# Optimization experiments

Hardware: AMD Instinct MI355X
Metric: run time of the kernel (lower is better)

The kernel has to match this reference:

```python
import jax, jax.numpy as jnp
import numpy as np

D = 1024           # input_size
D2 = 2 * D         # hidden width of the three inner linears
OUT = 1024         # output_size
S = 8192           # tokens per example


def setup_inputs() -> dict:
    key = jax.random.key(0)
    ks = jax.random.split(key, 11)
    def lin(k, fan_in, fan_out):
        bound = 1.0 / np.sqrt(fan_in)
        kw, kb = jax.random.split(k)
        W = jax.random.uniform(kw, (fan_in, fan_out), jnp.float32, -bound, bound)
        b = jax.random.uniform(kb, (fan_out,), jnp.float32, -bound, bound)
        return W, b
    W_in, b_in = lin(ks[0], D, D2)      # reading_example_input
    W_out, b_out = lin(ks[1], D, D2)    # reading_example_output
    W_cat, b_cat = lin(ks[2], D2, D2)   # concatenated_layer_map
    W_fin, b_fin = lin(ks[3], D2, OUT)  # final_map
    return {
        "input_embedding": jax.random.normal(ks[4], (1, S, D), jnp.float32),
        "output_embedding": jax.random.normal(ks[5], (1, S, D), jnp.float32),
        "random_augmentation": jax.random.normal(ks[6], (1, S, D), jnp.float32),
        "W_in": W_in, "b_in": b_in,
        "W_out": W_out, "b_out": b_out,
        "W_cat": W_cat, "b_cat": b_cat,
        "W_fin": W_fin, "b_fin": b_fin,
    }


def reference(input_embedding, output_embedding, random_augmentation,
              W_in, b_in, W_out, b_out, W_cat, b_cat, W_fin, b_fin):
    def march(x, y):
        # x, y: [1, S, D]
        iq = jax.nn.softmax(x @ W_in + b_in, axis=-1)[0]    # [S, 2D]
        oq = jax.nn.softmax(y @ W_out + b_out, axis=-1)[0]  # [S, 2D]
        cat = jnp.concatenate((x, y), axis=-1)[0]           # [S, 2D]
        icm = jax.nn.softmax(cat @ W_cat + b_cat, axis=-1)  # [S, 2D]
        iqk = iq.T @ icm                                    # [2D, 2D]
        oqk = oq.T @ icm                                    # [2D, 2D]
        meta = jax.nn.relu(iqk @ oqk.T)                     # [2D, 2D]
        scale = jnp.sqrt(jnp.float32(icm.shape[-1]))
        res = (icm @ meta) / scale                          # [S, 2D]
        return jax.nn.relu(res @ W_fin + b_fin)             # [S, OUT]

    transformation = march(input_embedding, output_embedding)
    random_desc = march(input_embedding, random_augmentation)
    return (transformation, random_desc)
```

## Files before the change

### kernel.cpp

```cpp
#include <hip/hip_runtime.h>

#define S_TOK 8192
#define DIM   1024
#define DIM2  2048
#define OUTN  1024

typedef __bf16 bf16x8 __attribute__((ext_vector_type(8)));
typedef float  f32x4  __attribute__((ext_vector_type(4)));
typedef short  s16x8  __attribute__((ext_vector_type(8)));
typedef unsigned short u16x4 __attribute__((ext_vector_type(4)));

__device__ __forceinline__ unsigned short f2bf(float x) {
  unsigned u = __builtin_bit_cast(unsigned, x);
  u = (u + 0x7FFFu + ((u >> 16) & 1u)) >> 16;
  return (unsigned short)u;
}
__device__ __forceinline__ float bf2f(unsigned short u) {
  return __builtin_bit_cast(float, (unsigned)u << 16);
}

__device__ __forceinline__ void gld_lds16(const void* g, void* l) {
  auto* g1 = reinterpret_cast<__attribute__((address_space(1))) unsigned*>(
      (unsigned long long)g);
  auto* l3 = reinterpret_cast<__attribute__((address_space(3))) unsigned*>(
      (unsigned long long)l);
  __builtin_amdgcn_global_load_lds(g1, l3, 16, 0, 0);
}

__device__ __forceinline__ int lds_off(int idx, int k) {
  int b = (idx << 7) + (k << 1);
  b ^= ((idx ^ (idx >> 3)) & 7) << 4;
  return b;
}

__global__ __launch_bounds__(256) void cvt_f32_bf16(const float* __restrict__ in,
                                                    unsigned short* __restrict__ out, int n4) {
  int i = blockIdx.x * 256 + threadIdx.x;
  if (i >= n4) return;
  float4 v = ((const float4*)in)[i];
  u16x4 o;
  o[0] = f2bf(v.x); o[1] = f2bf(v.y); o[2] = f2bf(v.z); o[3] = f2bf(v.w);
  *(u16x4*)(out + (size_t)i * 4) = o;
}

template <int F32IN>
__global__ __launch_bounds__(256) void transpose_to_bf16(const void* __restrict__ in,
                                                         unsigned short* __restrict__ out,
                                                         int R, int C) {
  __shared__ unsigned short t[64 * 64];
  const int r0 = blockIdx.y << 6, c0 = blockIdx.x << 6;
  const int tid = threadIdx.x;
#pragma unroll
  for (int i = 0; i < 2; ++i) {
    int ch = tid + (i << 8);
    int r = ch >> 3, c8 = (ch & 7) << 3;
    s16x8 w;
    if (F32IN) {
      const float* p = (const float*)in + (size_t)(r0 + r) * C + c0 + c8;
      float4 a = *(const float4*)p, b = *(const float4*)(p + 4);
      w[0] = (short)f2bf(a.x); w[1] = (short)f2bf(a.y);
      w[2] = (short)f2bf(a.z); w[3] = (short)f2bf(a.w);
      w[4] = (short)f2bf(b.x); w[5] = (short)f2bf(b.y);
      w[6] = (short)f2bf(b.z); w[7] = (short)f2bf(b.w);
    } else {
      w = *(const s16x8*)((const unsigned short*)in + (size_t)(r0 + r) * C + c0 + c8);
    }
    int sw = ((r ^ (r >> 3)) & 7) << 3;
    *(s16x8*)&t[(r << 6) + (c8 ^ sw)] = w;
  }
  __syncthreads();
#pragma unroll
  for (int i = 0; i < 2; ++i) {
    int ch = tid + (i << 8);
    int c = ch >> 3, r8 = (ch & 7) << 3;
    s16x8 w;
#pragma unroll
    for (int j = 0; j < 8; ++j) {
      int rr = r8 + j;
      w[j] = (short)t[(rr << 6) + (c ^ (((rr ^ (rr >> 3)) & 7) << 3))];
    }
    *(s16x8*)(out + (size_t)(c0 + c) * R + r0 + r8) = w;
  }
}

struct SmTab { unsigned short* T[6]; };
__global__ __launch_bounds__(512) void softmax_cols(SmTab tab) {
  unsigned short* T = tab.T[blockIdx.y];
  const int tid = threadIdx.x;
  const int colg = tid & 63, seg = tid >> 6;
  const size_t c = ((size_t)blockIdx.x << 6) + colg;
  float m = -1e30f, s = 0.f;
  for (int n = seg; n < DIM2; n += 8) {
    float v = bf2f(T[(size_t)n * S_TOK + c]);
    float mn = fmaxf(m, v);
    s = s * __expf(m - mn) + __expf(v - mn);
    m = mn;
  }
  __shared__ float redm[512], reds[512];
  redm[tid] = m; reds[tid] = s;
  __syncthreads();
  if (seg == 0) {
    float M = m, S = s;
#pragma unroll
    for (int k = 1; k < 8; ++k) {
      float mk = redm[colg + (k << 6)], sk = reds[colg + (k << 6)];
      float mn = fmaxf(M, mk);
      S = S * __expf(M - mn) + sk * __expf(mk - mn);
      M = mn;
    }
    redm[colg] = M; reds[colg] = 1.0f / S;
  }
  __syncthreads();
  m = redm[colg];
  const float inv = reds[colg];
  for (int n = seg; n < DIM2; n += 8) {
    size_t idx = (size_t)n * S_TOK + c;
    T[idx] = f2bf(__expf(bf2f(T[idx]) - m) * inv);
  }
}

struct GPtr {
  const unsigned short* A[3];
  const unsigned short* Arow2[3];
  const unsigned short* B[3];
  const unsigned short* Bk2[3];
  const float* bias[3];
  void* C[3];
};
template <int ASPLIT, int BSPLIT, int BIAS_ROW, int OUT_BF16>
__global__ __launch_bounds__(256, 3) void gemm_nt(GPtr p, int lda, int ldb, int ldc,
                                                  int K, float scale, int do_relu) {
  __shared__ char lds[32768];
  char* As = lds;
  char* Bs = lds + 16384;
  const int z = blockIdx.z;
  const int tid  = threadIdx.x;
  const int lane = tid & 63;
  const int wave = tid >> 6;
  const int wm = (wave >> 1) << 6;
  const int wn = (wave & 1) << 6;
  const int m0 = blockIdx.y << 7;
  const int n0 = blockIdx.x << 7;

  const unsigned short* Au = p.A[z];
  int mb = m0;
  if (ASPLIT && m0 >= 2048) { Au = p.Arow2[z]; mb = m0 - 2048; }
  const unsigned short* B  = p.B[z];
  const unsigned short* B2 = BSPLIT ? p.Bk2[z] : B;
  const float* bias = p.bias[z];
  void* Cv = p.C[z];

  int srow[4], sgk[4];
#pragma unroll
  for (int i = 0; i < 4; ++i) {
    int c = (wave << 8) + (i << 6) + lane;
    int row = c >> 3, kc = c & 7;
    srow[i] = row;
    sgk[i]  = (kc ^ ((row ^ (row >> 3)) & 7)) << 3;
  }

  f32x4 acc[4][4];
#pragma unroll
  for (int i = 0; i < 4; ++i)
#pragma unroll
    for (int j = 0; j < 4; ++j) acc[i][j] = {0.f, 0.f, 0.f, 0.f};

  for (int k0 = 0; k0 < K; k0 += 64) {
    const unsigned short* bsrc = B;
    int kb = k0;
    if (BSPLIT && k0 >= DIM) { bsrc = B2; kb = k0 - DIM; }
#pragma unroll
    for (int i = 0; i < 4; ++i) {
      char* dA = As + (((wave << 2) + i) << 10);
      char* dB = Bs + (((wave << 2) + i) << 10);
      gld_lds16(Au   + (size_t)(mb + srow[i]) * lda + k0 + sgk[i], dA);
      gld_lds16(bsrc + (size_t)(n0 + srow[i]) * ldb + kb + sgk[i], dB);
    }
    __syncthreads();
#pragma unroll
    for (int ks = 0; ks < 2; ++ks) {
      bf16x8 af[4], bfr[4];
      int kk = (ks << 5) + ((lane >> 4) << 3);
#pragma unroll
      for (int t = 0; t < 4; ++t) {
        af[t]  = *(const bf16x8*)(As + lds_off(wm + (t << 4) + (lane & 15), kk));
        bfr[t] = *(const bf16x8*)(Bs + lds_off(wn + (t << 4) + (lane & 15), kk));
      }
#pragma unroll
      for (int mt = 0; mt < 4; ++mt)
#pragma unroll
        for (int nt = 0; nt < 4; ++nt)
          acc[mt][nt] = __builtin_amdgcn_mfma_f32_16x16x32_bf16(af[mt], bfr[nt], acc[mt][nt], 0, 0, 0);
    }
    __syncthreads();
  }

#pragma unroll
  for (int nt = 0; nt < 4; ++nt) {
    int col = n0 + wn + (nt << 4) + (lane & 15);
    float bcol = (!BIAS_ROW && bias) ? bias[col] : 0.0f;
#pragma unroll
    for (int mt = 0; mt < 4; ++mt) {
      f32x4 a = acc[mt][nt];
#pragma unroll
      for (int r = 0; r < 4; ++r) {
        int rowg = m0 + wm + (mt << 4) + ((lane >> 4) << 2) + r;
        float bv = BIAS_ROW ? (bias ? bias[rowg] : 0.0f) : bcol;
        float v = a[r] * scale + bv;
        if (do_relu) v = fmaxf(v, 0.0f);
        if (OUT_BF16) ((unsigned short*)Cv)[(size_t)rowg * ldc + col] = f2bf(v);
        else          ((float*)Cv)[(size_t)rowg * ldc + col] = v;
      }
    }
  }
}

extern "C" void kernel_launch(void* const* d_in, const int* in_sizes, int n_in,
                              void* d_out, int out_size, void* d_ws, size_t ws_size,
                              hipStream_t stream) {
  const float* X   = (const float*)d_in[0];
  const float* Y   = (const float*)d_in[1];
  const float* R   = (const float*)d_in[2];
  const float* Wi  = (const float*)d_in[3];
  const float* bi  = (const float*)d_in[4];
  const float* Wo  = (const float*)d_in[5];
  const float* bo  = (const float*)d_in[6];
  const float* Wc  = (const float*)d_in[7];
  const float* bc  = (const float*)d_in[8];
  const float* Wf  = (const float*)d_in[9];
  const float* bf_ = (const float*)d_in[10];
  float* out = (float*)d_out;

  char* ws = (char*)d_ws;
  size_t off = 0;
  auto alloc = [&](size_t b) { char* p = ws + off; off += (b + 255) & ~(size_t)255; return p; };
  unsigned short* Xb   = (unsigned short*)alloc((size_t)S_TOK * DIM  * 2);
  unsigned short* Yb   = (unsigned short*)alloc((size_t)S_TOK * DIM  * 2);
  unsigned short* Rb   = (unsigned short*)alloc((size_t)S_TOK * DIM  * 2);
  unsigned short* WiT  = (unsigned short*)alloc((size_t)DIM2 * DIM  * 2);
  unsigned short* WoT  = (unsigned short*)alloc((size_t)DIM2 * DIM  * 2);
  unsigned short* WcT  = (unsigned short*)alloc((size_t)DIM2 * DIM2 * 2);
  unsigned short* WfT  = (unsigned short*)alloc((size_t)OUTN * DIM2 * 2);
  unsigned short* iqT  = (unsigned short*)alloc((size_t)DIM2 * S_TOK * 2);
  unsigned short* oqT0 = (unsigned short*)alloc((size_t)DIM2 * S_TOK * 2);
  unsigned short* oqT1 = (unsigned short*)alloc((size_t)DIM2 * S_TOK * 2);
  unsigned short* icmT0= (unsigned short*)alloc((size_t)DIM2 * S_TOK * 2);
  unsigned short* icmT1= (unsigned short*)alloc((size_t)DIM2 * S_TOK * 2);
  unsigned short* iqk0 = Xb;
  unsigned short* oqk0 = Xb + (size_t)DIM2*DIM2;
  unsigned short* iqk1 = Yb;
  unsigned short* oqk1 = Yb + (size_t)DIM2*DIM2;
  unsigned short* meta0= iqT;
  unsigned short* meta1= iqT + (size_t)DIM2*DIM2;
  unsigned short* MWT0 = iqT + (size_t)2*DIM2*DIM2;
  unsigned short* MWT1 = iqT + (size_t)2*DIM2*DIM2 + (size_t)OUTN*DIM2;
  unsigned short* icm0 = oqT0;
  unsigned short* icm1 = oqT1;

  auto cvt = [&](const float* s, unsigned short* d, int n) {
    int n4 = n >> 2;
    cvt_f32_bf16<<<dim3((n4 + 255) / 256), dim3(256), 0, stream>>>(s, d, n4);
  };
  cvt(X, Xb, S_TOK * DIM);
  cvt(Y, Yb, S_TOK * DIM);
  cvt(R, Rb, S_TOK * DIM);
  transpose_to_bf16<1><<<dim3(DIM2 / 64, DIM  / 64), 256, 0, stream>>>(Wi, WiT, DIM,  DIM2);
  transpose_to_bf16<1><<<dim3(DIM2 / 64, DIM  / 64), 256, 0, stream>>>(Wo, WoT, DIM,  DIM2);
  transpose_to_bf16<1><<<dim3(DIM2 / 64, DIM2 / 64), 256, 0, stream>>>(Wc, WcT, DIM2, DIM2);
  transpose_to_bf16<1><<<dim3(OUTN / 64, DIM2 / 64), 256, 0, stream>>>(Wf, WfT, DIM2, OUTN);

  const float rscale = 0.022097086912079608f;

  {
    GPtr g{};
    g.A[0] = WiT; g.A[1] = WoT; g.A[2] = WoT;
    g.B[0] = Xb;  g.B[1] = Yb;  g.B[2] = Rb;
    g.bias[0] = bi; g.bias[1] = bo; g.bias[2] = bo;
    g.C[0] = iqT; g.C[1] = oqT0; g.C[2] = oqT1;
    gemm_nt<0,0,1,1><<<dim3(S_TOK/128, DIM2/128, 3), 256, 0, stream>>>(
        g, DIM, DIM, S_TOK, DIM, 1.f, 0);
  }
  {
    GPtr g{};
    g.A[0] = WcT; g.A[1] = WcT;
    g.B[0] = Xb;  g.B[1] = Xb;
    g.Bk2[0] = Yb; g.Bk2[1] = Rb;
    g.bias[0] = bc; g.bias[1] = bc;
    g.C[0] = icmT0; g.C[1] = icmT1;
    gemm_nt<0,1,1,1><<<dim3(S_TOK/128, DIM2/128, 2), 256, 0, stream>>>(
        g, DIM2, DIM, S_TOK, DIM2, 1.f, 0);
  }
  {
    SmTab st{};
    st.T[0] = iqT; st.T[1] = oqT0; st.T[2] = oqT1; st.T[3] = icmT0; st.T[4] = icmT1;
    softmax_cols<<<dim3(S_TOK / 64, 5), dim3(512), 0, stream>>>(st);
  }
  {
    GPtr g{};
    g.A[0] = iqT; g.A[1] = iqT;
    g.Arow2[0] = oqT0; g.Arow2[1] = oqT1;
    g.B[0] = icmT0; g.B[1] = icmT1;
    g.C[0] = iqk0; g.C[1] = iqk1;
    gemm_nt<1,0,0,1><<<dim3(DIM2/128, 4096/128, 2), 256, 0, stream>>>(
        g, S_TOK, S_TOK, DIM2, S_TOK, 1.f, 0);
  }
  transpose_to_bf16<0><<<dim3(S_TOK / 64, DIM2 / 64), 256, 0, stream>>>(icmT0, icm0, DIM2, S_TOK);
  transpose_to_bf16<0><<<dim3(S_TOK / 64, DIM2 / 64), 256, 0, stream>>>(icmT1, icm1, DIM2, S_TOK);
  {
    GPtr g{};
    g.A[0] = iqk0; g.A[1] = iqk1;
    g.B[0] = oqk0; g.B[1] = oqk1;
    g.C[0] = meta0; g.C[1] = meta1;
    gemm_nt<0,0,0,1><<<dim3(DIM2/128, DIM2/128, 2), 256, 0, stream>>>(
        g, DIM2, DIM2, DIM2, DIM2, 1.f, 1);
  }
  {
    GPtr g{};
    g.A[0] = WfT; g.A[1] = WfT;
    g.B[0] = meta0; g.B[1] = meta1;
    g.C[0] = MWT0; g.C[1] = MWT1;
    gemm_nt<0,0,0,1><<<dim3(DIM2/128, OUTN/128, 2), 256, 0, stream>>>(
        g, DIM2, DIM2, DIM2, DIM2, rscale, 0);
  }
  {
    GPtr g{};
    g.A[0] = icm0; g.A[1] = icm1;
    g.B[0] = MWT0; g.B[1] = MWT1;
    g.bias[0] = bf_; g.bias[1] = bf_;
    g.C[0] = out; g.C[1] = out + (size_t)S_TOK * OUTN;
    gemm_nt<0,0,0,0><<<dim3(OUTN/128, S_TOK/128, 2), 256, 0, stream>>>(
        g, DIM2, DIM2, OUTN, DIM2, 1.f, 1);
  }
  (void)in_sizes; (void)n_in; (void)out_size; (void)ws_size;
}
```

Baseline: 993.7 us.

## Add 256x256-tile double-buffered GEMM kernel for the large matmuls

Adds a new gemm256 kernel: 512 threads computing a 256x256 output tile, a 64-wide K step double-buffered in 128KB of LDS with async global-to-LDS loads, explicit vmcnt waits and barriers, setprio around the MFMA blocks, and an XCD-aware remap of block ids. The four big GEMMs (projections, concat map, iqk/oqk, final) now use it instead of the 128x128 gemm_nt. The aim is more data reuse per LDS byte, and overlap of loads with MFMA. In exchange it carries much higher register and LDS pressure, and some grids get smaller (e.g. 8x16x2 blocks), which may hurt occupancy.

```diff
diff --git a/kernel.cpp b/kernel.cpp
--- a/kernel.cpp
+++ b/kernel.cpp
@@ -127,6 +127,7 @@
   const float* bias[3];
   void* C[3];
 };
+
 template <int ASPLIT, int BSPLIT, int BIAS_ROW, int OUT_BF16>
 __global__ __launch_bounds__(256, 3) void gemm_nt(GPtr p, int lda, int ldb, int ldc,
                                                   int K, float scale, int do_relu) {
@@ -205,6 +206,129 @@
 #pragma unroll
       for (int r = 0; r < 4; ++r) {
         int rowg = m0 + wm + (mt << 4) + ((lane >> 4) << 2) + r;
+        float bv = BIAS_ROW ? (bias ? bias[rowg] : 0.0f) : bcol;
+        float v = a[r] * scale + bv;
+        if (do_relu) v = fmaxf(v, 0.0f);
+        if (OUT_BF16) ((unsigned short*)Cv)[(size_t)rowg * ldc + col] = f2bf(v);
+        else          ((float*)Cv)[(size_t)rowg * ldc + col] = v;
+      }
+    }
+  }
+}
+
+template <int ASPLIT, int BSPLIT, int BIAS_ROW, int OUT_BF16>
+__global__ __launch_bounds__(512, 2) void gemm256(GPtr p, int lda, int ldb, int ldc,
+                                                  int K, float scale, int do_relu) {
+  __shared__ char lds[131072];
+  const int z = blockIdx.z;
+  const int tid  = threadIdx.x;
+  const int lane = tid & 63;
+  const int wave = tid >> 6;
+  const int wm   = wave >> 2;
+  const int wn   = wave & 3;
+
+  const int gx = gridDim.x;
+  const int nwg = gx * gridDim.y;
+  int id = blockIdx.y * gx + blockIdx.x;
+  id = (id & 7) * (nwg >> 3) + (id >> 3);
+  const int n0 = (id % gx) << 8;
+  const int m0 = (id / gx) << 8;
+
+  const unsigned short* Au = p.A[z];
+  int mb = m0;
+  if (ASPLIT && m0 >= 2048) { Au = p.Arow2[z]; mb = m0 - 2048; }
+  const unsigned short* Bp = p.B[z];
+  const unsigned short* B2 = BSPLIT ? p.Bk2[z] : Bp;
+  const float* bias = p.bias[z];
+  void* Cv = p.C[z];
+
+  int srow[4], sgk[4];
+#pragma unroll
+  for (int i = 0; i < 4; ++i) {
+    int c = (i << 9) + tid;
+    int row = c >> 3, kc = c & 7;
+    srow[i] = row;
+    sgk[i]  = (kc ^ ((row ^ (row >> 3)) & 7)) << 3;
+  }
+
+  auto stage = [&](int t) {
+    const int k0 = t << 6;
+    char* Abase = lds + ((t & 1) << 16);
+    char* Bbase = Abase + 32768;
+    const unsigned short* bsrc = Bp;
+    int kb = k0;
+    if (BSPLIT && k0 >= DIM) { bsrc = B2; kb = k0 - DIM; }
+#pragma unroll
+    for (int i = 0; i < 4; ++i) {
+      gld_lds16(Au   + (size_t)(mb + srow[i]) * lda + k0 + sgk[i],
+                Abase + (i << 13) + (wave << 10));
+      gld_lds16(bsrc + (size_t)(n0 + srow[i]) * ldb + kb + sgk[i],
+                Bbase + (i << 13) + (wave << 10));
+    }
+  };
+
+  f32x4 acc[8][4];
+#pragma unroll
+  for (int i = 0; i < 8; ++i)
+#pragma unroll
+    for (int j = 0; j < 4; ++j) acc[i][j] = {0.f, 0.f, 0.f, 0.f};
+
+  const int NT = K >> 6;
+  stage(0);
+  stage(1);
+
+  for (int t = 0; t < NT; ++t) {
+    if (t + 1 < NT) asm volatile("s_waitcnt vmcnt(8)" ::: "memory");
+    else            asm volatile("s_waitcnt vmcnt(0)" ::: "memory");
+    __builtin_amdgcn_s_barrier();
+    __builtin_amdgcn_sched_barrier(0);
+    const char* Ab = lds + ((t & 1) << 16);
+    const char* Bb = Ab + 32768;
+#pragma unroll
+    for (int half = 0; half < 2; ++half) {
+      const int kk = (half << 5) + ((lane >> 4) << 3);
+      bf16x8 aq[4], bq[4];
+#pragma unroll
+      for (int nf = 0; nf < 4; ++nf)
+        bq[nf] = *(const bf16x8*)(Bb + lds_off((wn << 6) + (nf << 4) + (lane & 15), kk));
+#pragma unroll
+      for (int mf = 0; mf < 4; ++mf)
+        aq[mf] = *(const bf16x8*)(Ab + lds_off((wm << 7) + (mf << 4) + (lane & 15), kk));
+      __builtin_amdgcn_s_setprio(1);
+#pragma unroll
+      for (int mf = 0; mf < 4; ++mf)
+#pragma unroll
+        for (int nf = 0; nf < 4; ++nf)
+          acc[mf][nf] = __builtin_amdgcn_mfma_f32_16x16x32_bf16(aq[mf], bq[nf], acc[mf][nf], 0, 0, 0);
+      __builtin_amdgcn_s_setprio(0);
+      __builtin_amdgcn_sched_barrier(0);
+#pragma unroll
+      for (int mf = 0; mf < 4; ++mf)
+        aq[mf] = *(const bf16x8*)(Ab + lds_off((wm << 7) + ((mf + 4) << 4) + (lane & 15), kk));
+      __builtin_amdgcn_s_setprio(1);
+#pragma unroll
+      for (int mf = 0; mf < 4; ++mf)
+#pragma unroll
+        for (int nf = 0; nf < 4; ++nf)
+          acc[mf + 4][nf] = __builtin_amdgcn_mfma_f32_16x16x32_bf16(aq[mf], bq[nf], acc[mf + 4][nf], 0, 0, 0);
+      __builtin_amdgcn_s_setprio(0);
+      __builtin_amdgcn_sched_barrier(0);
+    }
+    __builtin_amdgcn_s_barrier();
+    __builtin_amdgcn_sched_barrier(0);
+    if (t + 2 < NT) stage(t + 2);
+  }
+
+#pragma unroll
+  for (int nf = 0; nf < 4; ++nf) {
+    int col = n0 + (wn << 6) + (nf << 4) + (lane & 15);
+    float bcol = (!BIAS_ROW && bias) ? bias[col] : 0.0f;
+#pragma unroll
+    for (int mf = 0; mf < 8; ++mf) {
+      f32x4 a = acc[mf][nf];
+#pragma unroll
+      for (int r = 0; r < 4; ++r) {
+        int rowg = m0 + (wm << 7) + (mf << 4) + ((lane >> 4) << 2) + r;
         float bv = BIAS_ROW ? (bias ? bias[rowg] : 0.0f) : bcol;
         float v = a[r] * scale + bv;
         if (do_relu) v = fmaxf(v, 0.0f);
@@ -277,7 +401,7 @@
     g.B[0] = Xb;  g.B[1] = Yb;  g.B[2] = Rb;
     g.bias[0] = bi; g.bias[1] = bo; g.bias[2] = bo;
     g.C[0] = iqT; g.C[1] = oqT0; g.C[2] = oqT1;
-    gemm_nt<0,0,1,1><<<dim3(S_TOK/128, DIM2/128, 3), 256, 0, stream>>>(
+    gemm256<0,0,1,1><<<dim3(S_TOK/256, DIM2/256, 3), 512, 0, stream>>>(
         g, DIM, DIM, S_TOK, DIM, 1.f, 0);
   }
   {
@@ -287,7 +411,7 @@
     g.Bk2[0] = Yb; g.Bk2[1] = Rb;
     g.bias[0] = bc; g.bias[1] = bc;
     g.C[0] = icmT0; g.C[1] = icmT1;
-    gemm_nt<0,1,1,1><<<dim3(S_TOK/128, DIM2/128, 2), 256, 0, stream>>>(
+    gemm256<0,1,1,1><<<dim3(S_TOK/256, DIM2/256, 2), 512, 0, stream>>>(
         g, DIM2, DIM, S_TOK, DIM2, 1.f, 0);
   }
   {
@@ -301,7 +425,7 @@
     g.Arow2[0] = oqT0; g.Arow2[1] = oqT1;
     g.B[0] = icmT0; g.B[1] = icmT1;
     g.C[0] = iqk0; g.C[1] = iqk1;
-    gemm_nt<1,0,0,1><<<dim3(DIM2/128, 4096/128, 2), 256, 0, stream>>>(
+    gemm256<1,0,0,1><<<dim3(DIM2/256, 4096/256, 2), 512, 0, stream>>>(
         g, S_TOK, S_TOK, DIM2, S_TOK, 1.f, 0);
   }
   transpose_to_bf16<0><<<dim3(S_TOK / 64, DIM2 / 64), 256, 0, stream>>>(icmT0, icm0, DIM2, S_TOK);
@@ -328,7 +452,7 @@
     g.B[0] = MWT0; g.B[1] = MWT1;
     g.bias[0] = bf_; g.bias[1] = bf_;
     g.C[0] = out; g.C[1] = out + (size_t)S_TOK * OUTN;
-    gemm_nt<0,0,0,0><<<dim3(OUTN/128, S_TOK/128, 2), 256, 0, stream>>>(
+    gemm256<0,0,0,0><<<dim3(OUTN/256, S_TOK/256, 2), 512, 0, stream>>>(
         g, DIM2, DIM2, OUTN, DIM2, 1.f, 1);
   }
   (void)in_sizes; (void)n_in; (void)out_size; (void)ws_size;
```

Result: faster. 967.7 us (-2.6%).
